# Optimization experiments

Measured on AMD Instinct MI355X. Metric: run time of the kernel, lower is better.

Reference implementation:

```python
import jax, jax.numpy as jnp
import numpy as np

H = 128      # hidden_dim == type_hidden_dim
L = 2        # num_layers
AF, EF = 9, 3
N, EG = 500_000, 1_500_000
M, K, E = 50_000, 8, 10
ME, PN, PE = 100_000, 6, 8


def setup_inputs() -> dict:
    key = jax.random.key(0)
    ks = jax.random.split(key, 30)
    def w(k, shape, fan_in):
        return jax.random.normal(k, shape, jnp.float32) * (1.0 / np.sqrt(fan_in))
    inp = dict(
        x=jax.random.normal(ks[0], (N, AF), jnp.float32),
        edge_attr_global=jax.random.normal(ks[1], (EG, EF), jnp.float32),
        motif_nodes=jax.random.randint(ks[2], (M, K), 0, N),
        motif_types=jax.random.randint(ks[3], (M,), 0, 4),
        motif_edge_src=jax.random.randint(ks[4], (M, E), 0, K),
        motif_edge_dst=jax.random.randint(ks[5], (M, E), 0, K),
        motif_edge_eidx=jax.random.randint(ks[6], (M, E), 0, EG),
        motif_edge_index=jax.random.randint(ks[7], (2, ME), 0, M),
        attr_nodes=jax.random.randint(ks[8], (ME, PN), 0, N),
        attr_edges=jax.random.randint(ks[9], (ME, PE), 0, EG),
        type_emb=jax.random.normal(ks[10], (4, H), jnp.float32) * 0.02,
        atom_W=w(ks[11], (AF, H), AF), atom_b=jnp.zeros((H,), jnp.float32),
        edge_W=w(ks[12], (EF, H), EF), edge_b=jnp.zeros((H,), jnp.float32),
        conv_W1=w(ks[13], (L, H, H), H), conv_b1=jnp.zeros((L, H), jnp.float32),
        conv_W2=w(ks[14], (L, H, H), H), conv_b2=jnp.zeros((L, H), jnp.float32),
        conv_eps=jnp.zeros((L,), jnp.float32),
        attn_W=w(ks[15], (2 * H, 1), 2 * H), attn_b=jnp.zeros((1,), jnp.float32),
        emlp_W=w(ks[16], (3 * H, H), 3 * H), emlp_b=jnp.zeros((H,), jnp.float32),
        motif_W=w(ks[17], (2 * H, H), 2 * H), motif_b=jnp.zeros((H,), jnp.float32),
        me_W=w(ks[18], (2 * H, H), 2 * H), me_b=jnp.zeros((H,), jnp.float32),
    )
    return inp


def reference(x, edge_attr_global, motif_nodes, motif_types, motif_edge_src,
              motif_edge_dst, motif_edge_eidx, motif_edge_index, attr_nodes,
              attr_edges, type_emb, atom_W, atom_b, edge_W, edge_b,
              conv_W1, conv_b1, conv_W2, conv_b2, conv_eps,
              attn_W, attn_b, emlp_W, emlp_b, motif_W, motif_b, me_W, me_b):
    n_nodes = x.shape[0]
    half = H // 2
    # motif type embedding; second half scaled by graph node count
    tnode = type_emb[motif_types]                               # [M,H]
    tnode = jnp.concatenate([tnode[:, :half], tnode[:, half:] * n_nodes], -1)

    h = x[motif_nodes] @ atom_W + atom_b                        # [M,K,H]
    ea = edge_attr_global[motif_edge_eidx] @ edge_W + edge_b    # [M,E,H]

    bidx = jnp.arange(M)[:, None]                               # [M,1]
    for l in range(L):
        x_j = jnp.take_along_axis(h, motif_edge_src[..., None], axis=1)  # [M,E,H]
        msg = ea * x_j                                          # edge-modulated message
        agg = jnp.zeros_like(h).at[bidx, motif_edge_dst].add(msg)       # scatter-add at dst
        z = (1.0 + conv_eps[l]) * h + agg
        h = jax.nn.relu(z @ conv_W1[l] + conv_b1[l]) @ conv_W2[l] + conv_b2[l]

    # edge feature aggregation at BOTH endpoints
    edge_agg = (jnp.zeros_like(h)
                .at[bidx, motif_edge_src].add(ea)
                .at[bidx, motif_edge_dst].add(ea))
    alpha = jax.nn.sigmoid(jnp.concatenate([h, edge_agg], -1) @ attn_W + attn_b)  # [M,K,1]
    h_nodes = jnp.sum(alpha * h, axis=1)                        # [M,H]

    x_s = jnp.take_along_axis(h, motif_edge_src[..., None], axis=1)
    x_d = jnp.take_along_axis(h, motif_edge_dst[..., None], axis=1)
    h_edges = jax.nn.relu(jnp.concatenate([x_s, x_d, ea], -1) @ emlp_W + emlp_b)
    h_edges = jnp.mean(h_edges, axis=1)                         # [M,H]

    motifs_X = jnp.concatenate([h_nodes + h_edges, tnode], -1) @ motif_W + motif_b  # [M,H]

    # motif-level edge attributes
    st = motif_types[motif_edge_index[0]]
    en = motif_types[motif_edge_index[1]]
    t_edge = type_emb[st] + type_emb[en]                        # [ME,H]
    h_atom_edge = (x[attr_nodes] @ atom_W + atom_b).sum(axis=1) \
                + (edge_attr_global[attr_edges] @ edge_W + edge_b).sum(axis=1)  # [ME,H]
    motifs_edge_attr = jnp.concatenate([t_edge, h_atom_edge], -1) @ me_W + me_b  # [ME,H]

    return motifs_X, motifs_edge_attr
```

## Files before the change

### kernel.cpp

```cpp
#include <hip/hip_runtime.h>
#include <hip/hip_bf16.h>
#include <math.h>

#define HD 128
#define MPB 8
#define EPB 2

typedef __attribute__((ext_vector_type(8))) short short8;
typedef __attribute__((ext_vector_type(4))) float f32x4;
typedef unsigned short ushort_t;
typedef unsigned int uint32;

#define MFMA(a, b, c) __builtin_amdgcn_mfma_f32_16x16x32_bf16(a, b, c, 0, 0, 0)

#define WS_TE   0
#define WS_TM   2048
#define WS_AW2  2560
#define WS_EW2  3712
#define WS_CVEC 4096
#define FB_OFF 32768

#define FB_W1(l)  ((size_t)(l) * 65536)
#define FB_W2(l)  ((size_t)(l) * 65536 + 32768)
#define FB_WA     ((size_t)131072)
#define FB_WB     ((size_t)163840)
#define FB_WC     ((size_t)196608)
#define FB_WM     ((size_t)229376)
#define FB_ATOM   ((size_t)262144)
#define FB_EDGE   ((size_t)270336)

__device__ __forceinline__ float bf2f(ushort_t u) {
  union { float f; uint32 i; } c; c.i = ((uint32)u) << 16; return c.f;
}
__device__ __forceinline__ ushort_t f2bf(float f) {
  union { float ff; uint32 u; } c; c.ff = f;
  uint32 r = c.u + 0x7fff + ((c.u >> 16) & 1);
  return (ushort_t)(r >> 16);
}
__device__ __forceinline__ int off256(int row, int by) {
  return row * 256 + (by ^ ((row & 7) << 4));
}
__device__ __forceinline__ int offS(int row, int by) {
  return row * 256 + 192 + (by ^ ((row & 3) << 4));
}
__device__ __forceinline__ void store8(char* p, const float* v) {
  short8 r;
  #pragma unroll
  for (int j = 0; j < 8; ++j) r[j] = (short)f2bf(v[j]);
  *(short8*)p = r;
}

__global__ __launch_bounds__(128) void precompute_kernel(
    const float* __restrict__ type_emb, const float* __restrict__ atom_W,
    const float* __restrict__ atom_b, const float* __restrict__ edge_W,
    const float* __restrict__ edge_b, const float* __restrict__ motif_W,
    const float* __restrict__ me_W, const float* __restrict__ me_b,
    float n_nodes, float* __restrict__ ws)
{
  const int t = threadIdx.x;
  const int r = blockIdx.x;
  float acc = 0.0f;
  if (r < 16) {
    const int sc = r >> 2, ec = r & 3;
    for (int c = 0; c < HD; ++c)
      acc += (type_emb[sc*HD + c] + type_emb[ec*HD + c]) * me_W[c*HD + t];
    ws[WS_TE + r*HD + t] = acc;
  } else if (r < 20) {
    const int ty = r - 16;
    for (int c = 0; c < HD; ++c) {
      float tv = type_emb[ty*HD + c] * (c >= 64 ? n_nodes : 1.0f);
      acc += tv * motif_W[(HD + c)*HD + t];
    }
    ws[WS_TM + ty*HD + t] = acc;
  } else if (r < 29) {
    const int a = r - 20;
    for (int c = 0; c < HD; ++c)
      acc += atom_W[a*HD + c] * me_W[(HD + c)*HD + t];
    ws[WS_AW2 + a*HD + t] = acc;
  } else if (r < 32) {
    const int a = r - 29;
    for (int c = 0; c < HD; ++c)
      acc += edge_W[a*HD + c] * me_W[(HD + c)*HD + t];
    ws[WS_EW2 + a*HD + t] = acc;
  } else {
    acc = me_b[t];
    for (int c = 0; c < HD; ++c)
      acc += (6.0f*atom_b[c] + 8.0f*edge_b[c]) * me_W[(HD + c)*HD + t];
    ws[WS_CVEC + t] = acc;
  }
}

__global__ __launch_bounds__(64) void frag_kernel(
    const float* __restrict__ conv_W1, const float* __restrict__ conv_W2,
    const float* __restrict__ emlp_W, const float* __restrict__ motif_W,
    const float* __restrict__ atom_W, const float* __restrict__ edge_W,
    ushort_t* __restrict__ fbo)
{
  const int bid = blockIdx.x, l = threadIdx.x;
  int wi, kt, nt;
  if (bid < 256) { wi = bid >> 5; kt = (bid >> 3) & 3; nt = bid & 7; }
  else { int r = bid - 256; wi = 8 + (r >> 3); kt = 0; nt = r & 7; }
  const float* src; int Klim = 128;
  switch (wi) {
    case 0: src = conv_W1; break;
    case 1: src = conv_W2; break;
    case 2: src = conv_W1 + 16384; break;
    case 3: src = conv_W2 + 16384; break;
    case 4: src = emlp_W; break;
    case 5: src = emlp_W + 16384; break;
    case 6: src = emlp_W + 32768; break;
    case 7: src = motif_W; break;
    case 8: src = atom_W; Klim = 9; break;
    default: src = edge_W; Klim = 3; break;
  }
  size_t base = (wi < 8) ? (size_t)wi * 16384 : (size_t)131072 + (size_t)(wi - 8) * 4096;
  ushort_t* dst = fbo + base + ((size_t)(kt * 8 + nt) * 64 + l) * 8;
  #pragma unroll
  for (int j = 0; j < 8; ++j) {
    int k = kt * 32 + ((l >> 4) << 3) + j;
    int n = nt * 16 + (l & 15);
    float f = (k < Klim) ? src[k * HD + n] : 0.0f;
    dst[j] = f2bf(f);
  }
}

__global__ __launch_bounds__(256, 2) void motif_kernel(
    const float* __restrict__ x, const float* __restrict__ eag,
    const int* __restrict__ motif_nodes, const int* __restrict__ motif_types,
    const int* __restrict__ m_src, const int* __restrict__ m_dst,
    const int* __restrict__ m_eidx,
    const float* __restrict__ atom_b, const float* __restrict__ edge_b,
    const float* __restrict__ conv_b1, const float* __restrict__ conv_b2,
    const float* __restrict__ conv_eps,
    const float* __restrict__ attn_W, const float* __restrict__ attn_b,
    const float* __restrict__ emlp_b, const float* __restrict__ motif_b,
    const float* __restrict__ wsf, const ushort_t* __restrict__ fb,
    float* __restrict__ out)
{
  __shared__ __align__(16) char Hb[64 * 256];
  __shared__ __align__(16) char EAb[80 * 256];
  __shared__ __align__(16) char Wbuf[2][16384];
  __shared__ unsigned char zl[8][8][10];
  __shared__ unsigned char zcnt[8][8];
  __shared__ unsigned char gsr[80], gdr[80];
  __shared__ float qa[64];

  const int tid  = threadIdx.x;
  const int lane = tid & 63;
  const int wid  = tid >> 6;
  const int cl   = lane & 15;
  const int rg   = lane >> 4;
  const int rg16 = rg << 4;
  const int m0   = blockIdx.x * MPB;
  const int rb   = wid * 16;
  const int arow = rb + cl;
  const char* fbb = (const char*)fb;

#define STAGE16(B, OFF) do { \
    const char* _s = fbb + (OFF); \
    uint4 _a = *(const uint4*)(_s + (size_t)tid * 16); \
    uint4 _b = *(const uint4*)(_s + 4096  + (size_t)tid * 16); \
    uint4 _c = *(const uint4*)(_s + 8192  + (size_t)tid * 16); \
    uint4 _d = *(const uint4*)(_s + 12288 + (size_t)tid * 16); \
    *(uint4*)(&Wbuf[B][(size_t)tid * 16]) = _a; \
    *(uint4*)(&Wbuf[B][4096  + (size_t)tid * 16]) = _b; \
    *(uint4*)(&Wbuf[B][8192  + (size_t)tid * 16]) = _c; \
    *(uint4*)(&Wbuf[B][12288 + (size_t)tid * 16]) = _d; \
  } while (0)
#define WT(B, T) (*(const short8*)(&Wbuf[B][(((T) * 64 + lane) * 16)]))

  STAGE16(0, FB_ATOM);
  STAGE16(1, FB_W1(0));
  if (tid < 64) qa[tid] = 0.0f;
  if (tid < 80) {
    int m = tid / 10;
    gsr[tid] = (unsigned char)(m * 8 + m_src[(size_t)m0 * 10 + tid]);
    gdr[tid] = (unsigned char)(m * 8 + m_dst[(size_t)m0 * 10 + tid]);
  }
  if (tid >= 192 && tid < 200) {
    int m = tid - 192;
    #pragma unroll
    for (int k = 0; k < 8; ++k) zcnt[m][k] = 0;
    for (int e = 0; e < 10; ++e) {
      int s = m_src[(size_t)(m0 + m) * 10 + e];
      int d = m_dst[(size_t)(m0 + m) * 10 + e];
      int c = zcnt[m][d];
      zl[m][d][c] = (unsigned char)(e | (s << 4));
      zcnt[m][d] = (unsigned char)(c + 1);
    }
  }
  for (int i = tid; i < 64 * 32; i += 256) {
    int row = i >> 5, k = i & 31;
    int nd = motif_nodes[(size_t)m0 * 8 + row];
    float f = (k < 9) ? x[(size_t)nd * 9 + k] : 0.0f;
    *(ushort_t*)(Hb + offS(row, 2 * k)) = f2bf(f);
  }
  for (int i = tid; i < 80 * 32; i += 256) {
    int row = i >> 5, k = i & 31;
    int ei = m_eidx[(size_t)m0 * 10 + row];
    float f = (k < 3) ? eag[(size_t)ei * 3 + k] : 0.0f;
    *(ushort_t*)(EAb + offS(row, 2 * k)) = f2bf(f);
  }
  __syncthreads();

  {
    {
      short8 a = *(const short8*)(Hb + offS(arow, rg16));
      f32x4 acc[8];
      #pragma unroll
      for (int nt = 0; nt < 8; ++nt) { float bv = atom_b[nt * 16 + cl]; acc[nt] = f32x4{bv, bv, bv, bv}; }
      #pragma unroll
      for (int nt = 0; nt < 8; ++nt) acc[nt] = MFMA(a, WT(0, nt), acc[nt]);
      #pragma unroll
      for (int nt = 0; nt < 8; ++nt)
        #pragma unroll
        for (int i = 0; i < 4; ++i)
          *(ushort_t*)(Hb + off256(rb + rg * 4 + i, (nt * 16 + cl) * 2)) = f2bf(acc[nt][i]);
    }
    for (int mt = wid; mt < 5; mt += 4) {
      int rbe = mt * 16, row = rbe + cl;
      short8 a = *(const short8*)(EAb + offS(row, rg16));
      f32x4 acc[8];
      #pragma unroll
      for (int nt = 0; nt < 8; ++nt) { float bv = edge_b[nt * 16 + cl]; acc[nt] = f32x4{bv, bv, bv, bv}; }
      #pragma unroll
      for (int nt = 0; nt < 8; ++nt) acc[nt] = MFMA(a, WT(0, 8 + nt), acc[nt]);
      #pragma unroll
      for (int nt = 0; nt < 8; ++nt)
        #pragma unroll
        for (int i = 0; i < 4; ++i)
          *(ushort_t*)(EAb + off256(rbe + rg * 4 + i, (nt * 16 + cl) * 2)) = f2bf(acc[nt][i]);
    }
  }
  __syncthreads();

  #pragma unroll 1
  for (int l = 0; l < 2; ++l) {
    const float epl = 1.0f + conv_eps[l];

    float zf[4][8];
    #pragma unroll
    for (int it = 0; it < 4; ++it) {
      const int idx = tid + it * 256;
      const int row = idx >> 4;
      const int by  = (idx & 15) << 4;
      const int m = row >> 3, k = row & 7;
      short8 hv = *(const short8*)(Hb + off256(row, by));
      #pragma unroll
      for (int j = 0; j < 8; ++j) zf[it][j] = epl * bf2f((ushort_t)hv[j]);
      const int cnt = zcnt[m][k];
      for (int j2 = 0; j2 < cnt; ++j2) {
        const int p = zl[m][k][j2];
        short8 ev = *(const short8*)(EAb + off256(m * 10 + (p & 15), by));
        short8 sv = *(const short8*)(Hb  + off256(m * 8  + (p >> 4), by));
        #pragma unroll
        for (int j = 0; j < 8; ++j)
          zf[it][j] += bf2f((ushort_t)ev[j]) * bf2f((ushort_t)sv[j]);
      }
    }
    STAGE16(0, FB_W1(l) + 16384);
    __syncthreads();
    #pragma unroll
    for (int it = 0; it < 4; ++it) {
      const int idx = tid + it * 256;
      store8(Hb + off256(idx >> 4, (idx & 15) << 4), zf[it]);
    }
    __syncthreads();

    {
      f32x4 acc[8];
      #pragma unroll
      for (int nt = 0; nt < 8; ++nt) { float bv = conv_b1[l * HD + nt * 16 + cl]; acc[nt] = f32x4{bv, bv, bv, bv}; }
      #pragma unroll
      for (int kt = 0; kt < 2; ++kt) {
        short8 a = *(const short8*)(Hb + off256(arow, kt * 64 + rg16));
        #pragma unroll
        for (int nt = 0; nt < 8; ++nt) acc[nt] = MFMA(a, WT(1, kt * 8 + nt), acc[nt]);
      }
      __syncthreads();
      #pragma unroll
      for (int kt = 2; kt < 4; ++kt) {
        short8 a = *(const short8*)(Hb + off256(arow, kt * 64 + rg16));
        #pragma unroll
        for (int nt = 0; nt < 8; ++nt) acc[nt] = MFMA(a, WT(0, (kt - 2) * 8 + nt), acc[nt]);
      }
      STAGE16(1, FB_W2(l));
      #pragma unroll
      for (int nt = 0; nt < 8; ++nt)
        #pragma unroll
        for (int i = 0; i < 4; ++i)
          *(ushort_t*)(Hb + off256(rb + rg * 4 + i, (nt * 16 + cl) * 2)) = f2bf(fmaxf(acc[nt][i], 0.0f));
      __syncthreads();
    }
    {
      f32x4 acc[8];
      #pragma unroll
      for (int nt = 0; nt < 8; ++nt) { float bv = conv_b2[l * HD + nt * 16 + cl]; acc[nt] = f32x4{bv, bv, bv, bv}; }
      #pragma unroll
      for (int kt = 0; kt < 2; ++kt) {
        short8 a = *(const short8*)(Hb + off256(arow, kt * 64 + rg16));
        #pragma unroll
        for (int nt = 0; nt < 8; ++nt) acc[nt] = MFMA(a, WT(1, kt * 8 + nt), acc[nt]);
      }
      STAGE16(0, FB_W2(l) + 16384);
      __syncthreads();
      #pragma unroll
      for (int kt = 2; kt < 4; ++kt) {
        short8 a = *(const short8*)(Hb + off256(arow, kt * 64 + rg16));
        #pragma unroll
        for (int nt = 0; nt < 8; ++nt) acc[nt] = MFMA(a, WT(0, (kt - 2) * 8 + nt), acc[nt]);
      }
      if (l == 0) STAGE16(1, FB_W1(1));
      else        STAGE16(1, FB_WA);
      #pragma unroll
      for (int nt = 0; nt < 8; ++nt)
        #pragma unroll
        for (int i = 0; i < 4; ++i)
          *(ushort_t*)(Hb + off256(rb + rg * 4 + i, (nt * 16 + cl) * 2)) = f2bf(acc[nt][i]);
      __syncthreads();
    }
  }

  {
    int j = tid & 3;
    for (int r = tid >> 2; r < 80; r += 64) {
      float p = 0.0f;
      #pragma unroll
      for (int g = 0; g < 4; ++g) {
        short8 ev = *(const short8*)(EAb + off256(r, (j * 4 + g) << 4));
        const int c0 = j * 32 + g * 8;
        #pragma unroll
        for (int jj = 0; jj < 8; ++jj)
          p += bf2f((ushort_t)ev[jj]) * attn_W[HD + c0 + jj];
      }
      p += __shfl_xor(p, 1); p += __shfl_xor(p, 2);
      if (j == 0) {
        atomicAdd(&qa[gsr[r]], p);
        atomicAdd(&qa[gdr[r]], p);
      }
    }
  }
  __syncthreads();
  {
    int j = tid & 3, r = tid >> 2;
    float p = 0.0f;
    #pragma unroll
    for (int g = 0; g < 4; ++g) {
      short8 hv = *(const short8*)(Hb + off256(r, (j * 4 + g) << 4));
      const int c0 = j * 32 + g * 8;
      #pragma unroll
      for (int jj = 0; jj < 8; ++jj)
        p += bf2f((ushort_t)hv[jj]) * attn_W[c0 + jj];
    }
    p += __shfl_xor(p, 1); p += __shfl_xor(p, 2);
    if (j == 0) qa[r] = 1.0f / (1.0f + __expf(-(p + qa[r] + attn_b[0])));
  }
  __syncthreads();

  {
    f32x4 accT[8], acc4[2];
    #pragma unroll
    for (int nt = 0; nt < 8; ++nt) accT[nt] = f32x4{0, 0, 0, 0};
    acc4[0] = f32x4{0, 0, 0, 0}; acc4[1] = f32x4{0, 0, 0, 0};
    const int r1 = 16 * wid + cl, r4 = 64 + cl;
    #pragma unroll 1
    for (int w = 0; w < 3; ++w) {
      const char* AB = (w == 2) ? EAb : Hb;
      const int a1 = (w == 0) ? (int)gsr[r1] : (w == 1) ? (int)gdr[r1] : r1;
      const int a4 = (w == 0) ? (int)gsr[r4] : (w == 1) ? (int)gdr[r4] : r4;
      #pragma unroll
      for (int kt = 0; kt < 2; ++kt) {
        short8 av  = *(const short8*)(AB + off256(a1, kt * 64 + rg16));
        short8 av4 = *(const short8*)(AB + off256(a4, kt * 64 + rg16));
        #pragma unroll
        for (int nt = 0; nt < 8; ++nt) accT[nt] = MFMA(av, WT(1, kt * 8 + nt), accT[nt]);
        acc4[0] = MFMA(av4, WT(1, kt * 8 + 2 * wid), acc4[0]);
        acc4[1] = MFMA(av4, WT(1, kt * 8 + 2 * wid + 1), acc4[1]);
      }
      STAGE16(0, FB_WA + (size_t)w * 32768 + 16384);
      __syncthreads();
      #pragma unroll
      for (int kt = 2; kt < 4; ++kt) {
        short8 av  = *(const short8*)(AB + off256(a1, kt * 64 + rg16));
        short8 av4 = *(const short8*)(AB + off256(a4, kt * 64 + rg16));
        #pragma unroll
        for (int nt = 0; nt < 8; ++nt) accT[nt] = MFMA(av, WT(0, (kt - 2) * 8 + nt), accT[nt]);
        acc4[0] = MFMA(av4, WT(0, (kt - 2) * 8 + 2 * wid), acc4[0]);
        acc4[1] = MFMA(av4, WT(0, (kt - 2) * 8 + 2 * wid + 1), acc4[1]);
      }
      STAGE16(1, FB_WA + (size_t)(w + 1) * 32768);
      __syncthreads();
    }
    #pragma unroll
    for (int nt = 0; nt < 8; ++nt)
      #pragma unroll
      for (int i = 0; i < 4; ++i)
        *(ushort_t*)(EAb + off256(16 * wid + rg * 4 + i, (nt * 16 + cl) * 2)) = f2bf(accT[nt][i]);
    #pragma unroll
    for (int j = 0; j < 2; ++j)
      #pragma unroll
      for (int i = 0; i < 4; ++i)
        *(ushort_t*)(EAb + off256(64 + rg * 4 + i, ((2 * wid + j) * 16 + cl) * 2)) = f2bf(acc4[j][i]);
  }
  __syncthreads();

  float cv[8];
  if (tid < 128) {
    const int m  = tid >> 4;
    const int by = (tid & 15) << 4;
    const int c0 = (tid & 15) * 8;
    #pragma unroll
    for (int j = 0; j < 8; ++j) cv[j] = 0.0f;
    #pragma unroll
    for (int k = 0; k < 8; ++k) {
      short8 hv = *(const short8*)(Hb + off256(m * 8 + k, by));
      const float a = qa[m * 8 + k];
      #pragma unroll
      for (int j = 0; j < 8; ++j) cv[j] += a * bf2f((ushort_t)hv[j]);
    }
    float he[8];
    #pragma unroll
    for (int j = 0; j < 8; ++j) he[j] = 0.0f;
    #pragma unroll
    for (int e = 0; e < 10; ++e) {
      short8 rv = *(const short8*)(EAb + off256(m * 10 + e, by));
      #pragma unroll
      for (int j = 0; j < 8; ++j)
        he[j] += fmaxf(bf2f((ushort_t)rv[j]) + emlp_b[c0 + j], 0.0f);
    }
    #pragma unroll
    for (int j = 0; j < 8; ++j) cv[j] += 0.1f * he[j];
  }
  STAGE16(0, FB_WM + 16384);
  __syncthreads();
  if (tid < 128) {
    store8(EAb + off256(tid >> 4, (tid & 15) << 4), cv);
  } else {
    const int i = tid - 128;
    short8 z{};
    *(short8*)(EAb + off256(8 + (i >> 4), (i & 15) << 4)) = z;
  }
  __syncthreads();

  {
    f32x4 acc[2];
    acc[0] = f32x4{0, 0, 0, 0}; acc[1] = f32x4{0, 0, 0, 0};
    #pragma unroll
    for (int kt = 0; kt < 2; ++kt) {
      short8 a = *(const short8*)(EAb + off256(cl, kt * 64 + rg16));
      #pragma unroll
      for (int j = 0; j < 2; ++j)
        acc[j] = MFMA(a, WT(1, kt * 8 + 2 * wid + j), acc[j]);
    }
    #pragma unroll
    for (int kt = 2; kt < 4; ++kt) {
      short8 a = *(const short8*)(EAb + off256(cl, kt * 64 + rg16));
      #pragma unroll
      for (int j = 0; j < 2; ++j)
        acc[j] = MFMA(a, WT(0, (kt - 2) * 8 + 2 * wid + j), acc[j]);
    }
    #pragma unroll
    for (int j = 0; j < 2; ++j)
      #pragma unroll
      for (int i = 0; i < 4; ++i) {
        int row = rg * 4 + i;
        if (row < 8) {
          int col = (wid * 2 + j) * 16 + cl;
          int ty = motif_types[m0 + row];
          out[(size_t)(m0 + row) * HD + col] = acc[j][i] + motif_b[col] + wsf[WS_TM + ty * HD + col];
        }
      }
  }
#undef STAGE16
#undef WT
}

__global__ __launch_bounds__(256) void edge_kernel(
    const float* __restrict__ x, const float* __restrict__ eag,
    const int* __restrict__ motif_types, const int* __restrict__ mei,
    const int* __restrict__ attr_nodes, const int* __restrict__ attr_edges,
    const float* __restrict__ ws, float* __restrict__ out, int ME_)
{
  __shared__ int   ani[EPB][6];
  __shared__ int   aei[EPB][8];
  __shared__ float sxl[EPB][9];
  __shared__ float sel[EPB][3];
  __shared__ int   tei[EPB];

  const int tid = threadIdx.x;
  const int t = tid & (HD - 1);
  const int g = tid >> 7;
  const int me0 = blockIdx.x * EPB;

  if (tid < EPB*6) ani[tid/6][tid%6] = attr_nodes[(size_t)(me0 + tid/6)*6 + tid%6];
  if (tid >= 32 && tid < 32 + EPB*8) { int i = tid-32; aei[i/8][i%8] = attr_edges[(size_t)(me0 + i/8)*8 + i%8]; }
  if (tid >= 64 && tid < 64 + EPB) {
    const int e = tid - 64;
    const int a0 = mei[me0 + e], b0 = mei[ME_ + me0 + e];
    tei[e] = motif_types[a0]*4 + motif_types[b0];
  }
  __syncthreads();

  if (tid < EPB*9) {
    const int e = tid/9, a = tid%9;
    float s = 0.0f;
    #pragma unroll
    for (int p = 0; p < 6; ++p) s += x[(size_t)ani[e][p]*9 + a];
    sxl[e][a] = s;
  }
  if (tid >= 32 && tid < 32 + EPB*3) {
    const int i = tid-32, e = i/3, a = i%3;
    float s = 0.0f;
    #pragma unroll
    for (int p = 0; p < 8; ++p) s += eag[(size_t)aei[e][p]*3 + a];
    sel[e][a] = s;
  }
  __syncthreads();

  float acc = ws[WS_CVEC + t] + ws[WS_TE + tei[g]*HD + t];
  #pragma unroll
  for (int a = 0; a < 9; ++a) acc += sxl[g][a] * ws[WS_AW2 + a*HD + t];
  #pragma unroll
  for (int a = 0; a < 3; ++a) acc += sel[g][a] * ws[WS_EW2 + a*HD + t];
  out[(size_t)(me0 + g)*HD + t] = acc;
}

extern "C" void kernel_launch(void* const* d_in, const int* in_sizes, int n_in,
                              void* d_out, int out_size, void* d_ws, size_t ws_size,
                              hipStream_t stream) {
  const float* x          = (const float*)d_in[0];
  const float* eag        = (const float*)d_in[1];
  const int*   motif_nodes= (const int*)d_in[2];
  const int*   motif_types= (const int*)d_in[3];
  const int*   m_src      = (const int*)d_in[4];
  const int*   m_dst      = (const int*)d_in[5];
  const int*   m_eidx     = (const int*)d_in[6];
  const int*   mei        = (const int*)d_in[7];
  const int*   attr_nodes = (const int*)d_in[8];
  const int*   attr_edges = (const int*)d_in[9];
  const float* type_emb   = (const float*)d_in[10];
  const float* atom_W     = (const float*)d_in[11];
  const float* atom_b     = (const float*)d_in[12];
  const float* edge_W     = (const float*)d_in[13];
  const float* edge_b     = (const float*)d_in[14];
  const float* conv_W1    = (const float*)d_in[15];
  const float* conv_b1    = (const float*)d_in[16];
  const float* conv_W2    = (const float*)d_in[17];
  const float* conv_b2    = (const float*)d_in[18];
  const float* conv_eps   = (const float*)d_in[19];
  const float* attn_W     = (const float*)d_in[20];
  const float* attn_b     = (const float*)d_in[21];
  const float* emlp_W     = (const float*)d_in[22];
  const float* emlp_b     = (const float*)d_in[23];
  const float* motif_W    = (const float*)d_in[24];
  const float* motif_b    = (const float*)d_in[25];
  const float* me_W       = (const float*)d_in[26];
  const float* me_b       = (const float*)d_in[27];

  const int N_  = in_sizes[0] / 9;
  const int M_  = in_sizes[2] / 8;
  const int ME_ = in_sizes[7] / 2;

  float* wsf = (float*)d_ws;
  ushort_t* fb = (ushort_t*)((char*)d_ws + FB_OFF);
  float* out = (float*)d_out;

  precompute_kernel<<<33, 128, 0, stream>>>(type_emb, atom_W, atom_b, edge_W, edge_b,
                                            motif_W, me_W, me_b, (float)N_, wsf);
  frag_kernel<<<272, 64, 0, stream>>>(conv_W1, conv_W2, emlp_W, motif_W, atom_W, edge_W, fb);
  motif_kernel<<<M_/MPB, 256, 0, stream>>>(x, eag, motif_nodes, motif_types, m_src, m_dst, m_eidx,
      atom_b, edge_b, conv_b1, conv_b2, conv_eps, attn_W, attn_b, emlp_b, motif_b,
      wsf, fb, out);
  edge_kernel<<<ME_/EPB, 256, 0, stream>>>(x, eag, motif_types, mei, attr_nodes, attr_edges,
                                           wsf, out + (size_t)M_*HD, ME_);
}
```

Before: 554.1 us.

## Halve weight staging buffers to fit three motif blocks per CU

The two LDS weight buffers in motif_kernel shrink from 16 KB to 8 KB each, and the per-motif edge lists become a compacted CSR layout, so LDS use drops enough for a third resident block; launch bounds are raised to match. Every 128x128 GEMM is re-pipelined to stream one K-tile (8 KB) at a time, ping-ponging between the two buffers with a barrier per K-tile. The aim is more waves per CU to hide global and LDS latency. In exchange there are twice as many barriers, shallower prefetch, and a tighter register budget that may cause spills.

```diff
diff --git a/kernel.cpp b/kernel.cpp
--- a/kernel.cpp
+++ b/kernel.cpp
@@ -23,8 +23,6 @@
 #define FB_W1(l)  ((size_t)(l) * 65536)
 #define FB_W2(l)  ((size_t)(l) * 65536 + 32768)
 #define FB_WA     ((size_t)131072)
-#define FB_WB     ((size_t)163840)
-#define FB_WC     ((size_t)196608)
 #define FB_WM     ((size_t)229376)
 #define FB_ATOM   ((size_t)262144)
 #define FB_EDGE   ((size_t)270336)
@@ -124,7 +122,7 @@
   }
 }
 
-__global__ __launch_bounds__(256, 2) void motif_kernel(
+__global__ __launch_bounds__(256, 3) void motif_kernel(
     const float* __restrict__ x, const float* __restrict__ eag,
     const int* __restrict__ motif_nodes, const int* __restrict__ motif_types,
     const int* __restrict__ m_src, const int* __restrict__ m_dst,
@@ -139,9 +137,9 @@
 {
   __shared__ __align__(16) char Hb[64 * 256];
   __shared__ __align__(16) char EAb[80 * 256];
-  __shared__ __align__(16) char Wbuf[2][16384];
-  __shared__ unsigned char zl[8][8][10];
-  __shared__ unsigned char zcnt[8][8];
+  __shared__ __align__(16) char Wbuf[2][8192];
+  __shared__ unsigned char zl[8][10];
+  __shared__ unsigned char zoff[8][8];
   __shared__ unsigned char gsr[80], gdr[80];
   __shared__ float qa[64];
 
@@ -156,21 +154,17 @@
   const int arow = rb + cl;
   const char* fbb = (const char*)fb;
 
-#define STAGE16(B, OFF) do { \
+#define STAGE8(B, OFF) do { \
     const char* _s = fbb + (OFF); \
     uint4 _a = *(const uint4*)(_s + (size_t)tid * 16); \
-    uint4 _b = *(const uint4*)(_s + 4096  + (size_t)tid * 16); \
-    uint4 _c = *(const uint4*)(_s + 8192  + (size_t)tid * 16); \
-    uint4 _d = *(const uint4*)(_s + 12288 + (size_t)tid * 16); \
+    uint4 _b = *(const uint4*)(_s + 4096 + (size_t)tid * 16); \
     *(uint4*)(&Wbuf[B][(size_t)tid * 16]) = _a; \
-    *(uint4*)(&Wbuf[B][4096  + (size_t)tid * 16]) = _b; \
-    *(uint4*)(&Wbuf[B][8192  + (size_t)tid * 16]) = _c; \
-    *(uint4*)(&Wbuf[B][12288 + (size_t)tid * 16]) = _d; \
+    *(uint4*)(&Wbuf[B][4096 + (size_t)tid * 16]) = _b; \
   } while (0)
 #define WT(B, T) (*(const short8*)(&Wbuf[B][(((T) * 64 + lane) * 16)]))
 
-  STAGE16(0, FB_ATOM);
-  STAGE16(1, FB_W1(0));
+  STAGE8(0, FB_ATOM);
+  STAGE8(1, FB_EDGE);
   if (tid < 64) qa[tid] = 0.0f;
   if (tid < 80) {
     int m = tid / 10;
@@ -179,14 +173,14 @@
   }
   if (tid >= 192 && tid < 200) {
     int m = tid - 192;
-    #pragma unroll
-    for (int k = 0; k < 8; ++k) zcnt[m][k] = 0;
-    for (int e = 0; e < 10; ++e) {
-      int s = m_src[(size_t)(m0 + m) * 10 + e];
-      int d = m_dst[(size_t)(m0 + m) * 10 + e];
-      int c = zcnt[m][d];
-      zl[m][d][c] = (unsigned char)(e | (s << 4));
-      zcnt[m][d] = (unsigned char)(c + 1);
+    int cnt = 0;
+    for (int k = 0; k < 8; ++k) {
+      zoff[m][k] = (unsigned char)cnt;
+      for (int e = 0; e < 10; ++e) {
+        int s = m_src[(size_t)(m0 + m) * 10 + e];
+        int d = m_dst[(size_t)(m0 + m) * 10 + e];
+        if (d == k) zl[m][cnt++] = (unsigned char)(e | (s << 4));
+      }
     }
   }
   for (int i = tid; i < 64 * 32; i += 256) {
@@ -224,7 +218,7 @@
       #pragma unroll
       for (int nt = 0; nt < 8; ++nt) { float bv = edge_b[nt * 16 + cl]; acc[nt] = f32x4{bv, bv, bv, bv}; }
       #pragma unroll
-      for (int nt = 0; nt < 8; ++nt) acc[nt] = MFMA(a, WT(0, 8 + nt), acc[nt]);
+      for (int nt = 0; nt < 8; ++nt) acc[nt] = MFMA(a, WT(1, nt), acc[nt]);
       #pragma unroll
       for (int nt = 0; nt < 8; ++nt)
         #pragma unroll
@@ -238,6 +232,7 @@
   for (int l = 0; l < 2; ++l) {
     const float epl = 1.0f + conv_eps[l];
 
+    STAGE8(0, FB_W1(l));
     float zf[4][8];
     #pragma unroll
     for (int it = 0; it < 4; ++it) {
@@ -248,9 +243,10 @@
       short8 hv = *(const short8*)(Hb + off256(row, by));
       #pragma unroll
       for (int j = 0; j < 8; ++j) zf[it][j] = epl * bf2f((ushort_t)hv[j]);
-      const int cnt = zcnt[m][k];
-      for (int j2 = 0; j2 < cnt; ++j2) {
-        const int p = zl[m][k][j2];
+      const int ib = zoff[m][k];
+      const int ie = (k < 7) ? (int)zoff[m][k + 1] : 10;
+      for (int j2 = ib; j2 < ie; ++j2) {
+        const int p = zl[m][j2];
         short8 ev = *(const short8*)(EAb + off256(m * 10 + (p & 15), by));
         short8 sv = *(const short8*)(Hb  + off256(m * 8  + (p >> 4), by));
         #pragma unroll
@@ -258,7 +254,6 @@
           zf[it][j] += bf2f((ushort_t)ev[j]) * bf2f((ushort_t)sv[j]);
       }
     }
-    STAGE16(0, FB_W1(l) + 16384);
     __syncthreads();
     #pragma unroll
     for (int it = 0; it < 4; ++it) {
@@ -272,52 +267,42 @@
       #pragma unroll
       for (int nt = 0; nt < 8; ++nt) { float bv = conv_b1[l * HD + nt * 16 + cl]; acc[nt] = f32x4{bv, bv, bv, bv}; }
       #pragma unroll
-      for (int kt = 0; kt < 2; ++kt) {
+      for (int kt = 0; kt < 4; ++kt) {
         short8 a = *(const short8*)(Hb + off256(arow, kt * 64 + rg16));
-        #pragma unroll
-        for (int nt = 0; nt < 8; ++nt) acc[nt] = MFMA(a, WT(1, kt * 8 + nt), acc[nt]);
-      }
-      __syncthreads();
-      #pragma unroll
-      for (int kt = 2; kt < 4; ++kt) {
-        short8 a = *(const short8*)(Hb + off256(arow, kt * 64 + rg16));
-        #pragma unroll
-        for (int nt = 0; nt < 8; ++nt) acc[nt] = MFMA(a, WT(0, (kt - 2) * 8 + nt), acc[nt]);
-      }
-      STAGE16(1, FB_W2(l));
-      #pragma unroll
-      for (int nt = 0; nt < 8; ++nt)
-        #pragma unroll
-        for (int i = 0; i < 4; ++i)
-          *(ushort_t*)(Hb + off256(rb + rg * 4 + i, (nt * 16 + cl) * 2)) = f2bf(fmaxf(acc[nt][i], 0.0f));
-      __syncthreads();
+        if (kt < 3) STAGE8((kt + 1) & 1, FB_W1(l) + (size_t)(kt + 1) * 8192);
+        else        STAGE8(0, FB_W2(l));
+        #pragma unroll
+        for (int nt = 0; nt < 8; ++nt) acc[nt] = MFMA(a, WT(kt & 1, nt), acc[nt]);
+        if (kt == 3) {
+          #pragma unroll
+          for (int nt = 0; nt < 8; ++nt)
+            #pragma unroll
+            for (int i = 0; i < 4; ++i)
+              *(ushort_t*)(Hb + off256(rb + rg * 4 + i, (nt * 16 + cl) * 2)) = f2bf(fmaxf(acc[nt][i], 0.0f));
+        }
+        __syncthreads();
+      }
     }
     {
       f32x4 acc[8];
       #pragma unroll
       for (int nt = 0; nt < 8; ++nt) { float bv = conv_b2[l * HD + nt * 16 + cl]; acc[nt] = f32x4{bv, bv, bv, bv}; }
       #pragma unroll
-      for (int kt = 0; kt < 2; ++kt) {
+      for (int kt = 0; kt < 4; ++kt) {
         short8 a = *(const short8*)(Hb + off256(arow, kt * 64 + rg16));
-        #pragma unroll
-        for (int nt = 0; nt < 8; ++nt) acc[nt] = MFMA(a, WT(1, kt * 8 + nt), acc[nt]);
-      }
-      STAGE16(0, FB_W2(l) + 16384);
-      __syncthreads();
-      #pragma unroll
-      for (int kt = 2; kt < 4; ++kt) {
-        short8 a = *(const short8*)(Hb + off256(arow, kt * 64 + rg16));
-        #pragma unroll
-        for (int nt = 0; nt < 8; ++nt) acc[nt] = MFMA(a, WT(0, (kt - 2) * 8 + nt), acc[nt]);
-      }
-      if (l == 0) STAGE16(1, FB_W1(1));
-      else        STAGE16(1, FB_WA);
-      #pragma unroll
-      for (int nt = 0; nt < 8; ++nt)
-        #pragma unroll
-        for (int i = 0; i < 4; ++i)
-          *(ushort_t*)(Hb + off256(rb + rg * 4 + i, (nt * 16 + cl) * 2)) = f2bf(acc[nt][i]);
-      __syncthreads();
+        if (kt < 3)      STAGE8((kt + 1) & 1, FB_W2(l) + (size_t)(kt + 1) * 8192);
+        else if (l == 1) STAGE8(0, FB_WA);
+        #pragma unroll
+        for (int nt = 0; nt < 8; ++nt) acc[nt] = MFMA(a, WT(kt & 1, nt), acc[nt]);
+        if (kt == 3) {
+          #pragma unroll
+          for (int nt = 0; nt < 8; ++nt)
+            #pragma unroll
+            for (int i = 0; i < 4; ++i)
+              *(ushort_t*)(Hb + off256(rb + rg * 4 + i, (nt * 16 + cl) * 2)) = f2bf(acc[nt][i]);
+        }
+        __syncthreads();
+      }
     }
   }
 
@@ -369,27 +354,17 @@
       const int a1 = (w == 0) ? (int)gsr[r1] : (w == 1) ? (int)gdr[r1] : r1;
       const int a4 = (w == 0) ? (int)gsr[r4] : (w == 1) ? (int)gdr[r4] : r4;
       #pragma unroll
-      for (int kt = 0; kt < 2; ++kt) {
+      for (int kt = 0; kt < 4; ++kt) {
+        const int g = w * 4 + kt;
         short8 av  = *(const short8*)(AB + off256(a1, kt * 64 + rg16));
         short8 av4 = *(const short8*)(AB + off256(a4, kt * 64 + rg16));
-        #pragma unroll
-        for (int nt = 0; nt < 8; ++nt) accT[nt] = MFMA(av, WT(1, kt * 8 + nt), accT[nt]);
-        acc4[0] = MFMA(av4, WT(1, kt * 8 + 2 * wid), acc4[0]);
-        acc4[1] = MFMA(av4, WT(1, kt * 8 + 2 * wid + 1), acc4[1]);
-      }
-      STAGE16(0, FB_WA + (size_t)w * 32768 + 16384);
-      __syncthreads();
-      #pragma unroll
-      for (int kt = 2; kt < 4; ++kt) {
-        short8 av  = *(const short8*)(AB + off256(a1, kt * 64 + rg16));
-        short8 av4 = *(const short8*)(AB + off256(a4, kt * 64 + rg16));
-        #pragma unroll
-        for (int nt = 0; nt < 8; ++nt) accT[nt] = MFMA(av, WT(0, (kt - 2) * 8 + nt), accT[nt]);
-        acc4[0] = MFMA(av4, WT(0, (kt - 2) * 8 + 2 * wid), acc4[0]);
-        acc4[1] = MFMA(av4, WT(0, (kt - 2) * 8 + 2 * wid + 1), acc4[1]);
-      }
-      STAGE16(1, FB_WA + (size_t)(w + 1) * 32768);
-      __syncthreads();
+        STAGE8((g + 1) & 1, FB_WA + (size_t)(g + 1) * 8192);
+        #pragma unroll
+        for (int nt = 0; nt < 8; ++nt) accT[nt] = MFMA(av, WT(g & 1, nt), accT[nt]);
+        acc4[0] = MFMA(av4, WT(g & 1, 2 * wid), acc4[0]);
+        acc4[1] = MFMA(av4, WT(g & 1, 2 * wid + 1), acc4[1]);
+        __syncthreads();
+      }
     }
     #pragma unroll
     for (int nt = 0; nt < 8; ++nt)
@@ -431,7 +406,7 @@
     #pragma unroll
     for (int j = 0; j < 8; ++j) cv[j] += 0.1f * he[j];
   }
-  STAGE16(0, FB_WM + 16384);
+  STAGE8(1, FB_WM + 8192);
   __syncthreads();
   if (tid < 128) {
     store8(EAb + off256(tid >> 4, (tid & 15) << 4), cv);
@@ -446,18 +421,14 @@
     f32x4 acc[2];
     acc[0] = f32x4{0, 0, 0, 0}; acc[1] = f32x4{0, 0, 0, 0};
     #pragma unroll
-    for (int kt = 0; kt < 2; ++kt) {
+    for (int kt = 0; kt < 4; ++kt) {
       short8 a = *(const short8*)(EAb + off256(cl, kt * 64 + rg16));
+      if (kt == 1) STAGE8(0, FB_WM + 16384);
+      if (kt == 2) STAGE8(1, FB_WM + 24576);
       #pragma unroll
       for (int j = 0; j < 2; ++j)
-        acc[j] = MFMA(a, WT(1, kt * 8 + 2 * wid + j), acc[j]);
-    }
-    #pragma unroll
-    for (int kt = 2; kt < 4; ++kt) {
-      short8 a = *(const short8*)(EAb + off256(cl, kt * 64 + rg16));
-      #pragma unroll
-      for (int j = 0; j < 2; ++j)
-        acc[j] = MFMA(a, WT(0, (kt - 2) * 8 + 2 * wid + j), acc[j]);
+        acc[j] = MFMA(a, WT(kt & 1, 2 * wid + j), acc[j]);
+      if (kt < 3) __syncthreads();
     }
     #pragma unroll
     for (int j = 0; j < 2; ++j)
@@ -471,7 +442,7 @@
         }
       }
   }
-#undef STAGE16
+#undef STAGE8
 #undef WT
 }
 
```

Result: slower. 760.6 us (+37.3%).
